# Kernel tuning notes

Hardware: AMD Instinct MI355X
Metric: run time of the kernel (lower is better)

Reference implementation:

```python
import jax, jax.numpy as jnp
import numpy as np

L, S, M, N, E, H = 1024, 1024, 256, 8, 512, 8


def embed_rotary(x, cos, sin):
    # x: [B, T, E]; interleaved rotate-half as in RotaryPositionEncoding.embed_rotary
    x2 = jnp.stack([-x[..., 1::2], x[..., 0::2]], axis=-1).reshape(x.shape)
    return x * cos + x2 * sin


def setup_inputs() -> dict:
    key = jax.random.key(0)
    ks = jax.random.split(key, 12)
    return {
        "query": jax.random.normal(ks[0], (L, N, E), jnp.float32),
        "key": jax.random.normal(ks[1], (S, N, E), jnp.float32),
        "value": jax.random.normal(ks[2], (S, N, E), jnp.float32),
        "in_proj_weight": jax.random.normal(ks[3], (3 * E, E), jnp.float32) / np.sqrt(E).astype(np.float32),
        "in_proj_bias": jnp.zeros((3 * E,), jnp.float32),
        "out_proj_weight": jax.random.normal(ks[4], (E, E), jnp.float32) / np.sqrt(E).astype(np.float32),
        "out_proj_bias": jnp.zeros((E,), jnp.float32),
        "rot_q": jax.random.normal(ks[5], (N, L, E, 2), jnp.float32),
        "rot_k": jax.random.normal(ks[6], (N, S, E, 2), jnp.float32),
        "k_mem": jax.random.normal(ks[7], (M, N, E), jnp.float32),
        "v_mem": jax.random.normal(ks[8], (M, N, E), jnp.float32),
        "gate_attn": jax.random.normal(ks[9], (H,), jnp.float32),
        "mem_mask": jax.random.randint(ks[10], (N, M), 0, 2).astype(bool),
        "num_heads": H,
    }


def reference(query, key, value, in_proj_weight, in_proj_bias, out_proj_weight,
              out_proj_bias, rot_q, rot_k, k_mem, v_mem, gate_attn, mem_mask, num_heads):
    L_, N_, E_ = query.shape
    S_ = key.shape[0]
    H_ = num_heads
    hd = E_ // H_
    scale = float(hd) ** -0.5
    # separate q/k/v projections (qkv not identical path)
    q = query @ in_proj_weight[:E_].T + in_proj_bias[:E_]
    k = key @ in_proj_weight[E_:2 * E_].T + in_proj_bias[E_:2 * E_]
    v = value @ in_proj_weight[2 * E_:].T + in_proj_bias[2 * E_:]
    q = q * scale
    # inline rotary PE (applied in batch-first layout, then back)
    q = embed_rotary(q.transpose(1, 0, 2), rot_q[..., 0], rot_q[..., 1]).transpose(1, 0, 2)
    k = embed_rotary(k.transpose(1, 0, 2), rot_k[..., 0], rot_k[..., 1]).transpose(1, 0, 2)
    qh = q.reshape(L_, N_, H_, hd).transpose(1, 2, 0, 3)  # [N,H,L,hd]
    kh = k.reshape(S_, N_, H_, hd).transpose(1, 2, 0, 3)  # [N,H,S,hd]
    vh = v.reshape(S_, N_, H_, hd).transpose(1, 2, 0, 3)
    scores = jnp.einsum('nhld,nhsd->nhls', qh, kh)
    # slot-competition: softmax over queries (slots), then renormalize over keys
    w = jax.nn.softmax(scores, axis=2) + 1e-8
    w = w / w.sum(axis=-1, keepdims=True)
    attn = jnp.einsum('nhls,nhsd->nhld', w, vh)
    # memorizing-transformer style memory K/V branch with sigmoid head gating
    Mm = k_mem.shape[0]
    km = k_mem.reshape(Mm, N_, H_, hd).transpose(1, 2, 0, 3)  # [N,H,M,hd]
    vm = v_mem.reshape(Mm, N_, H_, hd).transpose(1, 2, 0, 3)
    sm = jnp.einsum('nhld,nhmd->nhlm', qh, km)
    sm = jnp.where(mem_mask[:, None, None, :], -1e9, sm)  # additive -inf mask
    wm = jax.nn.softmax(sm, axis=-1)
    om = jnp.einsum('nhlm,nhmd->nhld', wm, vm)
    gate = jax.nn.sigmoid(gate_attn)[None, :, None, None]  # [1,H,1,1]
    attn = gate * om + (1.0 - gate) * attn
    out = attn.transpose(2, 0, 1, 3).reshape(L_, N_, E_)  # back to [L,N,E]
    return out @ out_proj_weight.T + out_proj_bias
```

## Files before the change

### kernel.cpp

```cpp
#include <hip/hip_runtime.h>
#include <hip/hip_bf16.h>

typedef __hip_bfloat16 bf16;
typedef __bf16 bf16x8 __attribute__((ext_vector_type(8)));
typedef float f32x4 __attribute__((ext_vector_type(4)));

#define LQ 1024
#define SK 1024
#define MMEM 256
#define NB 8
#define EE 512
#define NH 8
#define HD 64
#define NBH 64

__device__ inline __bf16 tobf(float f) {
  __hip_bfloat16 h = __float2bfloat16(f);
  return *reinterpret_cast<__bf16*>(&h);
}
__device__ inline float bf2f(__bf16 x) {
  unsigned short u; __builtin_memcpy(&u, &x, 2);
  unsigned int v = (unsigned int)u << 16;
  float f; __builtin_memcpy(&f, &v, 4);
  return f;
}
__device__ inline f32x4 MFMA(bf16x8 a, bf16x8 b, f32x4 c) {
  return __builtin_amdgcn_mfma_f32_16x16x32_bf16(a, b, c, 0, 0, 0);
}

__device__ inline void gload_lds16(const bf16* g, void* l) {
  __builtin_amdgcn_global_load_lds(
      (const __attribute__((address_space(1))) void*)g,
      (__attribute__((address_space(3))) void*)l, 16, 0, 0);
}

__device__ inline bf16x8 load8(const float* p) {
  float4 a = *(const float4*)p;
  float4 b = *(const float4*)(p + 4);
  bf16x8 r;
  r[0] = tobf(a.x); r[1] = tobf(a.y); r[2] = tobf(a.z); r[3] = tobf(a.w);
  r[4] = tobf(b.x); r[5] = tobf(b.y); r[6] = tobf(b.z); r[7] = tobf(b.w);
  return r;
}

#define CVT_T0 524288
#define CVT_T3 98304
#define CVT_T4 32768
__global__ __launch_bounds__(256) void convert5(
    const float* __restrict__ q, const float* __restrict__ k,
    const float* __restrict__ v, const float* __restrict__ w,
    const float* __restrict__ o, bf16* __restrict__ qc, bf16* __restrict__ kc,
    bf16* __restrict__ vc, bf16* __restrict__ wc, bf16* __restrict__ oc)
{
  long long t = (long long)blockIdx.x * 256 + threadIdx.x;
  const float* src; bf16* dst; long long idx;
  if (t < CVT_T0)               { src = q; dst = qc; idx = t; }
  else if (t < 2 * CVT_T0)      { src = k; dst = kc; idx = t - CVT_T0; }
  else if (t < 3 * CVT_T0)      { src = v; dst = vc; idx = t - 2 * CVT_T0; }
  else if (t < 3 * CVT_T0 + CVT_T3) { src = w; dst = wc; idx = t - 3 * CVT_T0; }
  else                          { src = o; dst = oc; idx = t - 3 * CVT_T0 - CVT_T3; }
  *(bf16x8*)(dst + idx * 8) = load8(src + idx * 8);
}

__global__ __launch_bounds__(256) void gemm_proj3(
    const bf16* __restrict__ qc, const bf16* __restrict__ kc,
    const bf16* __restrict__ vc, const bf16* __restrict__ ipwb,
    const float* __restrict__ ipb, bf16* __restrict__ pq,
    bf16* __restrict__ pk, bf16* __restrict__ v_raw)
{
  __shared__ __align__(16) char smem[33792];
  __bf16* As = (__bf16*)smem;
  __bf16* Bs = (__bf16*)(smem + 16384);
  const int z = blockIdx.z;
  const bf16* A = (z == 0) ? qc : (z == 1) ? kc : vc;
  const bf16* W = ipwb + (long long)z * EE * EE;
  const float* bias = ipb + z * EE;
  const float alpha = (z == 0) ? 0.125f : 1.f;
  const int bid2 = blockIdx.y * gridDim.x + blockIdx.x;
  const int xcd = bid2 & 7, sub = bid2 >> 3;
  const int by = (xcd << 3) + (sub >> 2);
  const int bx = sub & 3;
  const int tm0 = by << 7, tn0 = bx << 7;
  const int t = threadIdx.x;
  const int wave = t >> 6, lane = t & 63;
  const int wrow0 = (wave & 1) << 6, wcol0 = (wave >> 1) << 6;
  const int m16 = lane & 15, quad = lane >> 4;

  const f32x4 zero = {0.f, 0.f, 0.f, 0.f};
  f32x4 acc[4][4];
#pragma unroll
  for (int mi = 0; mi < 4; ++mi)
#pragma unroll
    for (int ni = 0; ni < 4; ++ni) acc[mi][ni] = zero;

  const bf16* Ab = A + (long long)tm0 * EE;
  const bf16* Bb = W + (long long)tn0 * EE;
  const int ob_u = wave << 10;

  for (int k0 = 0; k0 < EE; k0 += 64) {
#pragma unroll
    for (int c = 0; c < 4; ++c) {
      int ob = (c << 12) + ob_u;
      int obl = ob + (lane << 4);
      int row = obl >> 7;
      int ce = (obl & 127) >> 1;
      gload_lds16(Ab + (long long)row * EE + k0 + ce, smem + ob);
      gload_lds16(Bb + (long long)row * EE + k0 + ce, smem + 16384 + ob);
    }
    __syncthreads();
#pragma unroll
    for (int kh = 0; kh < 2; ++kh) {
      bf16x8 av[4], bv[4];
#pragma unroll
      for (int i = 0; i < 4; ++i) {
        av[i] = *(bf16x8*)(As + ((wrow0 + (i << 4) + m16) << 6) + (kh << 5) + (quad << 3));
        bv[i] = *(bf16x8*)(Bs + ((wcol0 + (i << 4) + m16) << 6) + (kh << 5) + (quad << 3));
      }
#pragma unroll
      for (int mi = 0; mi < 4; ++mi)
#pragma unroll
        for (int ni = 0; ni < 4; ++ni)
          acc[mi][ni] = MFMA(av[mi], bv[ni], acc[mi][ni]);
    }
    __syncthreads();
  }

  __bf16 (*Cs)[132] = (__bf16(*)[132])smem;
#pragma unroll
  for (int mi = 0; mi < 4; ++mi)
#pragma unroll
    for (int ni = 0; ni < 4; ++ni) {
      int col = wcol0 + (ni << 4) + m16;
      float bv = bias[tn0 + col];
#pragma unroll
      for (int r = 0; r < 4; ++r)
        Cs[wrow0 + (mi << 4) + (quad << 2) + r][col] =
            tobf((acc[mi][ni][r] + bv) * alpha);
    }
  __syncthreads();
  bf16* O = (z == 0) ? pq : (z == 1) ? pk : v_raw;
  const int crow = t >> 1, ch0 = (t & 1) << 6;
  long long gb = (long long)(tm0 + crow) * EE + tn0 + ch0;
#pragma unroll
  for (int j = 0; j < 64; j += 8)
    *(uint4*)(O + gb + j) = *(uint4*)&Cs[crow][ch0 + j];
}

__global__ __launch_bounds__(256) void rotary_kernel(
    const bf16* __restrict__ pq, const bf16* __restrict__ pk,
    const float* __restrict__ rot_q, const float* __restrict__ rot_k,
    bf16* __restrict__ Qh, bf16* __restrict__ Kh)
{
  const bf16* src = blockIdx.y ? pk : pq;
  const float* rot = blockIdx.y ? rot_k : rot_q;
  bf16* dst = blockIdx.y ? Kh : Qh;
  const int t = threadIdx.x;
  const int row = (blockIdx.x << 2) + (t >> 6);
  const int e0 = (t & 63) << 3;
  const int l = row >> 3, n = row & 7;
  bf16x8 x = *(const bf16x8*)(src + (long long)row * EE + e0);
  const float* rp = rot + ((((long long)n * LQ + l) * EE + e0) << 1);
  __bf16 vals[8];
#pragma unroll
  for (int j = 0; j < 8; j += 2) {
    float4 cs4 = *(const float4*)(rp + (j << 1));
    float x0 = bf2f(x[j]);
    float x1 = bf2f(x[j + 1]);
    vals[j]     = tobf(x0 * cs4.x - x1 * cs4.y);
    vals[j + 1] = tobf(x1 * cs4.z + x0 * cs4.w);
  }
  const int h = e0 >> 6, d0 = e0 & 63;
  *(uint4*)(dst + (((long long)(n * NH + h) * LQ + l) * HD + d0)) = *(uint4*)vals;
}

__global__ __launch_bounds__(256) void colsum_kernel(
    const bf16* __restrict__ Qh, const bf16* __restrict__ Kh,
    float* __restrict__ csum)
{
  __shared__ __align__(16) __bf16 Ks[64][72];
  __shared__ __align__(16) __bf16 Qd[2][64][72];
  __shared__ float cpart[64][2];
  const int bid = blockIdx.y * gridDim.x + blockIdx.x;
  const int xcd = bid & 7, sub = bid >> 3;
  const int b = (xcd << 3) + (sub >> 4);
  const int st0 = (sub & 15) << 6;
  const int t = threadIdx.x;
  const int lrow = t >> 2, lcol = (t & 3) << 4;
  const int wave = t >> 6, lane = t & 63;
  const int wm = (wave & 1) << 5, wn = (wave >> 1) << 5;
  const int m16 = lane & 15, quad = lane >> 4;

  const bf16* qbase = Qh + ((long long)b * LQ + lrow) * HD + lcol;
  {
    const bf16* kp = Kh + ((long long)b * SK + st0 + lrow) * HD + lcol;
    *(bf16x8*)&Ks[lrow][lcol] = *(const bf16x8*)kp;
    *(bf16x8*)&Ks[lrow][lcol + 8] = *(const bf16x8*)(kp + 8);
    *(bf16x8*)&Qd[0][lrow][lcol] = *(const bf16x8*)qbase;
    *(bf16x8*)&Qd[0][lrow][lcol + 8] = *(const bf16x8*)(qbase + 8);
  }
  __syncthreads();
  bf16x8 bk[2][2];
#pragma unroll
  for (int ni = 0; ni < 2; ++ni)
#pragma unroll
    for (int kh = 0; kh < 2; ++kh)
      bk[ni][kh] = *(bf16x8*)&Ks[wn + (ni << 4) + m16][(kh << 5) + (quad << 3)];

  const f32x4 zero = {0.f, 0.f, 0.f, 0.f};
  float colp[2] = {0.f, 0.f};
  int cur = 0;
  for (int lt = 0; lt < 16; ++lt) {
    bf16x8 qr0, qr1;
    if (lt < 15) {
      const bf16* qp = qbase + (long long)((lt + 1) << 6) * HD;
      qr0 = *(const bf16x8*)qp;
      qr1 = *(const bf16x8*)(qp + 8);
    }
    f32x4 s00 = zero, s01 = zero, s10 = zero, s11 = zero;
    __builtin_amdgcn_s_setprio(1);
#pragma unroll
    for (int kh = 0; kh < 2; ++kh) {
      bf16x8 a0 = *(bf16x8*)&Qd[cur][wm + m16][(kh << 5) + (quad << 3)];
      bf16x8 a1 = *(bf16x8*)&Qd[cur][wm + 16 + m16][(kh << 5) + (quad << 3)];
      s00 = MFMA(a0, bk[0][kh], s00);
      s01 = MFMA(a0, bk[1][kh], s01);
      s10 = MFMA(a1, bk[0][kh], s10);
      s11 = MFMA(a1, bk[1][kh], s11);
    }
    __builtin_amdgcn_s_setprio(0);
    f32x4 sacc[2][2] = {{s00, s01}, {s10, s11}};
#pragma unroll
    for (int mi = 0; mi < 2; ++mi)
#pragma unroll
      for (int ni = 0; ni < 2; ++ni)
#pragma unroll
        for (int r = 0; r < 4; ++r)
          colp[ni] += __expf(sacc[mi][ni][r]);
    if (lt < 15) {
      *(bf16x8*)&Qd[cur ^ 1][lrow][lcol] = qr0;
      *(bf16x8*)&Qd[cur ^ 1][lrow][lcol + 8] = qr1;
    }
    __syncthreads();
    cur ^= 1;
  }
  for (int ni = 0; ni < 2; ++ni) {
    float v = colp[ni];
    v += __shfl_down(v, 32, 64);
    v += __shfl_down(v, 16, 64);
    if (quad == 0) cpart[wn + (ni << 4) + m16][wm >> 5] = v;
  }
  __syncthreads();
  if (t < 64) csum[b * SK + st0 + t] = cpart[t][0] + cpart[t][1];
}

__global__ __launch_bounds__(256) void vsum_kernel(
    const bf16* __restrict__ Vt, float* __restrict__ Vsum)
{
  int wid = blockIdx.x * 4 + (threadIdx.x >> 6);
  int lane = threadIdx.x & 63;
  const bf16* p = Vt + (long long)wid * SK + lane * 16;
  float s = 0.f;
  bf16x8 v0 = *(const bf16x8*)p;
  bf16x8 v1 = *(const bf16x8*)(p + 8);
#pragma unroll
  for (int j = 0; j < 8; ++j) s += bf2f(v0[j]) + bf2f(v1[j]);
  for (int off = 32; off; off >>= 1) s += __shfl_down(s, off, 64);
  if (lane == 0) Vsum[wid] = s;
}

__global__ __launch_bounds__(256) void attn_fused(
    const bf16* __restrict__ Qh, const bf16* __restrict__ Kh,
    const bf16* __restrict__ Vt, const bf16* __restrict__ km,
    const bf16* __restrict__ vmt, const float* __restrict__ csum,
    const float* __restrict__ Vsum, const int* __restrict__ mask,
    const float* __restrict__ gate, bf16* __restrict__ comb)
{
  __shared__ __align__(16) __bf16 Kd[2][64][72];
  __shared__ __align__(16) __bf16 Vd[2][64][72];
  __shared__ __align__(16) __bf16 Ps[4096];
  __shared__ __align__(16) float rcs[SK];
  __shared__ __align__(16) float mskf[MMEM];
  __shared__ float rpa[64][2];
  __shared__ float rpm[64][2];
  const int bid = blockIdx.y * gridDim.x + blockIdx.x;
  const int xcd = bid & 7, sub = bid >> 3;
  const int b = (xcd << 3) + (sub >> 4);
  const int tm0 = (sub & 15) << 6;
  const int n = b >> 3, h = b & 7;
  const int t = threadIdx.x;
  const int lrow = t >> 2, lcol = (t & 3) << 4;
  const int wave = t >> 6, lane = t & 63;
  const int wm = (wave & 1) << 5, wn = (wave >> 1) << 5;
  const int m16 = lane & 15, quad = lane >> 4;
  const int swz = (m16 & 7) << 4;

#pragma unroll
  for (int i = 0; i < 4; ++i)
    rcs[t + i * 256] = 1.f / csum[b * SK + t + i * 256];
  mskf[t] = mask[n * MMEM + t] ? 0.f : 1.f;
  {
    const bf16* qp = Qh + ((long long)b * LQ + tm0 + lrow) * HD + lcol;
    *(bf16x8*)&Kd[0][lrow][lcol] = *(const bf16x8*)qp;
    *(bf16x8*)&Kd[0][lrow][lcol + 8] = *(const bf16x8*)(qp + 8);
  }
  __syncthreads();
  bf16x8 aq[2][2];
#pragma unroll
  for (int li = 0; li < 2; ++li)
#pragma unroll
    for (int kh = 0; kh < 2; ++kh)
      aq[li][kh] = *(bf16x8*)&Kd[0][wm + (li << 4) + m16][(kh << 5) + (quad << 3)];

  const bf16* kbase_m = km + ((long long)b * MMEM + lrow) * HD + lcol;
  const bf16* vbase_m = vmt + ((long long)b * HD + lrow) * MMEM + lcol;
  {
    bf16x8 k0 = *(const bf16x8*)kbase_m;
    bf16x8 k1 = *(const bf16x8*)(kbase_m + 8);
    bf16x8 v0 = *(const bf16x8*)vbase_m;
    bf16x8 v1 = *(const bf16x8*)(vbase_m + 8);
    *(bf16x8*)&Kd[1][lrow][lcol] = k0;
    *(bf16x8*)&Kd[1][lrow][lcol + 8] = k1;
    *(bf16x8*)&Vd[1][lrow][lcol] = v0;
    *(bf16x8*)&Vd[1][lrow][lcol + 8] = v1;
  }
  __syncthreads();

  const f32x4 zero = {0.f, 0.f, 0.f, 0.f};
  f32x4 m00 = zero, m01 = zero, m10 = zero, m11 = zero;
  float rsm[2] = {0.f, 0.f};
  int cur = 1;
  for (int mt = 0; mt < 4; ++mt) {
    bf16x8 kr0, kr1, vr0, vr1;
    if (mt < 3) {
      const bf16* kp = kbase_m + (long long)((mt + 1) << 6) * HD;
      const bf16* vp = vbase_m + ((mt + 1) << 6);
      kr0 = *(const bf16x8*)kp;
      kr1 = *(const bf16x8*)(kp + 8);
      vr0 = *(const bf16x8*)vp;
      vr1 = *(const bf16x8*)(vp + 8);
    }
    f32x4 s00 = zero, s01 = zero, s10 = zero, s11 = zero;
    __builtin_amdgcn_s_setprio(1);
#pragma unroll
    for (int kh = 0; kh < 2; ++kh) {
      bf16x8 ak0 = *(bf16x8*)&Kd[cur][wn + m16][(kh << 5) + (quad << 3)];
      bf16x8 ak1 = *(bf16x8*)&Kd[cur][wn + 16 + m16][(kh << 5) + (quad << 3)];
      s00 = MFMA(ak0, aq[0][kh], s00);
      s01 = MFMA(ak0, aq[1][kh], s01);
      s10 = MFMA(ak1, aq[0][kh], s10);
      s11 = MFMA(ak1, aq[1][kh], s11);
    }
    __builtin_amdgcn_s_setprio(0);
    {
      char* pA = (char*)Ps + (wm + m16) * 128;
      char* pB = (char*)Ps + (wm + 16 + m16) * 128;
#pragma unroll
      for (int si = 0; si < 2; ++si) {
        int sloc = wn + (si << 4) + (quad << 2);
        f32x4 mf4 = *(const f32x4*)&mskf[(mt << 6) + sloc];
        f32x4 sA = si ? s10 : s00;
        f32x4 sB = si ? s11 : s01;
        __bf16 vA[4], vB[4];
#pragma unroll
        for (int r = 0; r < 4; ++r) {
          float pa = __expf(sA[r]) * mf4[r];
          rsm[0] += pa; vA[r] = tobf(pa);
          float pb = __expf(sB[r]) * mf4[r];
          rsm[1] += pb; vB[r] = tobf(pb);
        }
        int sbyte = (sloc << 1) ^ swz;
        *(uint2*)(pA + sbyte) = *(uint2*)vA;
        *(uint2*)(pB + sbyte) = *(uint2*)vB;
      }
    }
    __syncthreads();
    if (mt < 3) {
      *(bf16x8*)&Kd[cur ^ 1][lrow][lcol] = kr0;
      *(bf16x8*)&Kd[cur ^ 1][lrow][lcol + 8] = kr1;
      *(bf16x8*)&Vd[cur ^ 1][lrow][lcol] = vr0;
      *(bf16x8*)&Vd[cur ^ 1][lrow][lcol + 8] = vr1;
    }
    __builtin_amdgcn_s_setprio(1);
#pragma unroll
    for (int kh = 0; kh < 2; ++kh) {
      int sb = (kh << 6) + (quad << 4);
      bf16x8 ap0 = *(bf16x8*)((char*)Ps + (wm + m16) * 128 + (sb ^ swz));
      bf16x8 ap1 = *(bf16x8*)((char*)Ps + (wm + 16 + m16) * 128 + (sb ^ swz));
      bf16x8 bv0 = *(bf16x8*)&Vd[cur][wn + m16][(kh << 5) + (quad << 3)];
      bf16x8 bv1 = *(bf16x8*)&Vd[cur][wn + 16 + m16][(kh << 5) + (quad << 3)];
      m00 = MFMA(ap0, bv0, m00);
      m01 = MFMA(ap0, bv1, m01);
      m10 = MFMA(ap1, bv0, m10);
      m11 = MFMA(ap1, bv1, m11);
    }
    __builtin_amdgcn_s_setprio(0);
    __syncthreads();
    cur ^= 1;
  }

  f32x4 o00 = zero, o01 = zero, o10 = zero, o11 = zero;
  float rsa[2] = {0.f, 0.f};
  const bf16* kbase = Kh + ((long long)b * SK + lrow) * HD + lcol;
  const bf16* vbase = Vt + ((long long)b * HD + lrow) * SK + lcol;
  {
    bf16x8 k0 = *(const bf16x8*)kbase;
    bf16x8 k1 = *(const bf16x8*)(kbase + 8);
    bf16x8 v0 = *(const bf16x8*)vbase;
    bf16x8 v1 = *(const bf16x8*)(vbase + 8);
    *(bf16x8*)&Kd[1][lrow][lcol] = k0;
    *(bf16x8*)&Kd[1][lrow][lcol + 8] = k1;
    *(bf16x8*)&Vd[1][lrow][lcol] = v0;
    *(bf16x8*)&Vd[1][lrow][lcol + 8] = v1;
  }
  __syncthreads();
  cur = 1;
  for (int st = 0; st < 16; ++st) {
    bf16x8 kr0, kr1, vr0, vr1;
    if (st < 15) {
      const bf16* kp = kbase + (long long)((st + 1) << 6) * HD;
      const bf16* vp = vbase + ((st + 1) << 6);
      kr0 = *(const bf16x8*)kp;
      kr1 = *(const bf16x8*)(kp + 8);
      vr0 = *(const bf16x8*)vp;
      vr1 = *(const bf16x8*)(vp + 8);
    }
    f32x4 s00 = zero, s01 = zero, s10 = zero, s11 = zero;
    __builtin_amdgcn_s_setprio(1);
#pragma unroll
    for (int kh = 0; kh < 2; ++kh) {
      bf16x8 ak0 = *(bf16x8*)&Kd[cur][wn + m16][(kh << 5) + (quad << 3)];
      bf16x8 ak1 = *(bf16x8*)&Kd[cur][wn + 16 + m16][(kh << 5) + (quad << 3)];
      s00 = MFMA(ak0, aq[0][kh], s00);
      s01 = MFMA(ak0, aq[1][kh], s01);
      s10 = MFMA(ak1, aq[0][kh], s10);
      s11 = MFMA(ak1, aq[1][kh], s11);
    }
    __builtin_amdgcn_s_setprio(0);
    {
      char* pA = (char*)Ps + (wm + m16) * 128;
      char* pB = (char*)Ps + (wm + 16 + m16) * 128;
#pragma unroll
      for (int si = 0; si < 2; ++si) {
        int sloc = wn + (si << 4) + (quad << 2);
        f32x4 rc4 = *(const f32x4*)&rcs[(st << 6) + sloc];
        f32x4 sA = si ? s10 : s00;
        f32x4 sB = si ? s11 : s01;
        __bf16 vA[4], vB[4];
#pragma unroll
        for (int r = 0; r < 4; ++r) {
          float pa = __expf(sA[r]) * rc4[r];
          rsa[0] += pa; vA[r] = tobf(pa);
          float pb = __expf(sB[r]) * rc4[r];
          rsa[1] += pb; vB[r] = tobf(pb);
        }
        int sbyte = (sloc << 1) ^ swz;
        *(uint2*)(pA + sbyte) = *(uint2*)vA;
        *(uint2*)(pB + sbyte) = *(uint2*)vB;
      }
    }
    __syncthreads();
    if (st < 15) {
      *(bf16x8*)&Kd[cur ^ 1][lrow][lcol] = kr0;
      *(bf16x8*)&Kd[cur ^ 1][lrow][lcol + 8] = kr1;
      *(bf16x8*)&Vd[cur ^ 1][lrow][lcol] = vr0;
      *(bf16x8*)&Vd[cur ^ 1][lrow][lcol + 8] = vr1;
    }
    __builtin_amdgcn_s_setprio(1);
#pragma unroll
    for (int kh = 0; kh < 2; ++kh) {
      int sb = (kh << 6) + (quad << 4);
      bf16x8 ap0 = *(bf16x8*)((char*)Ps + (wm + m16) * 128 + (sb ^ swz));
      bf16x8 ap1 = *(bf16x8*)((char*)Ps + (wm + 16 + m16) * 128 + (sb ^ swz));
      bf16x8 bv0 = *(bf16x8*)&Vd[cur][wn + m16][(kh << 5) + (quad << 3)];
      bf16x8 bv1 = *(bf16x8*)&Vd[cur][wn + 16 + m16][(kh << 5) + (quad << 3)];
      o00 = MFMA(ap0, bv0, o00);
      o01 = MFMA(ap0, bv1, o01);
      o10 = MFMA(ap1, bv0, o10);
      o11 = MFMA(ap1, bv1, o11);
    }
    __builtin_amdgcn_s_setprio(0);
    __syncthreads();
    cur ^= 1;
  }

#pragma unroll
  for (int li = 0; li < 2; ++li) {
    float va = rsa[li];
    va += __shfl_xor(va, 16, 64);
    va += __shfl_xor(va, 32, 64);
    float vm = rsm[li];
    vm += __shfl_xor(vm, 16, 64);
    vm += __shfl_xor(vm, 32, 64);
    if (quad == 0) {
      rpa[wm + (li << 4) + m16][wn >> 5] = va;
      rpm[wm + (li << 4) + m16][wn >> 5] = vm;
    }
  }
  __syncthreads();

  const float* vs = Vsum + b * HD;
  const float g = 1.f / (1.f + __expf(-gate[h]));
  f32x4 oacc[2][2] = {{o00, o01}, {o10, o11}};
  f32x4 macc[2][2] = {{m00, m01}, {m10, m11}};
  for (int mi = 0; mi < 2; ++mi)
    for (int ni = 0; ni < 2; ++ni) {
      int col = wn + (ni << 4) + m16;
      float vsc = 1e-8f * vs[col];
      for (int r = 0; r < 4; ++r) {
        int row = wm + (mi << 4) + (quad << 2) + r;
        float ra = rpa[row][0] + rpa[row][1];
        float rm = rpm[row][0] + rpm[row][1];
        float oa = (oacc[mi][ni][r] + vsc) / (ra + (float)SK * 1e-8f);
        float om = macc[mi][ni][r] / rm;
        Kd[0][row][col] = tobf(g * om + (1.f - g) * oa);
      }
    }
  __syncthreads();
  uint4 u0 = *(uint4*)&Kd[0][lrow][lcol];
  uint4 u1 = *(uint4*)&Kd[0][lrow][lcol + 8];
  long long gb = ((long long)b * LQ + tm0 + lrow) * HD + lcol;
  *(uint4*)(comb + gb) = u0;
  *(uint4*)(comb + gb + 8) = u1;
}

__global__ __launch_bounds__(256) void gemm_out(
    const bf16* __restrict__ comb, const bf16* __restrict__ opwb,
    const float* __restrict__ opb, float* __restrict__ out)
{
  __shared__ __align__(16) char smem[32768];
  __bf16* As = (__bf16*)smem;
  __bf16* Bs = (__bf16*)(smem + 16384);
  const int bid2 = blockIdx.y * gridDim.x + blockIdx.x;
  const int xcd = bid2 & 7, sub = bid2 >> 3;
  const int by = (xcd << 3) + (sub >> 2);
  const int bx = sub & 3;
  const int tm0 = by << 7, tn0 = bx << 7;
  const int t = threadIdx.x;
  const int wave = t >> 6, lane = t & 63;
  const int wrow0 = (wave & 1) << 6, wcol0 = (wave >> 1) << 6;
  const int m16 = lane & 15, quad = lane >> 4;

  const f32x4 zero = {0.f, 0.f, 0.f, 0.f};
  f32x4 acc[4][4];
#pragma unroll
  for (int mi = 0; mi < 4; ++mi)
#pragma unroll
    for (int ni = 0; ni < 4; ++ni) acc[mi][ni] = zero;

  const bf16* Bb = opwb + (long long)tn0 * EE;
  const int ob_u = wave << 10;

  for (int k0 = 0; k0 < EE; k0 += 64) {
    const int h = k0 >> 6;
#pragma unroll
    for (int c = 0; c < 4; ++c) {
      int ob = (c << 12) + ob_u;
      int obl = ob + (lane << 4);
      int row = obl >> 7;
      int ce = (obl & 127) >> 1;
      int arow = tm0 + row;
      int l = arow >> 3, nn = arow & 7;
      gload_lds16(comb + (((long long)(nn * NH + h) * LQ + l) * HD + ce),
                  smem + ob);
      gload_lds16(Bb + (long long)row * EE + k0 + ce, smem + 16384 + ob);
    }
    __syncthreads();
#pragma unroll
    for (int kh = 0; kh < 2; ++kh) {
      bf16x8 av[4], bv[4];
#pragma unroll
      for (int i = 0; i < 4; ++i) {
        av[i] = *(bf16x8*)(As + ((wrow0 + (i << 4) + m16) << 6) + (kh << 5) + (quad << 3));
        bv[i] = *(bf16x8*)(Bs + ((wcol0 + (i << 4) + m16) << 6) + (kh << 5) + (quad << 3));
      }
#pragma unroll
      for (int mi = 0; mi < 4; ++mi)
#pragma unroll
        for (int ni = 0; ni < 4; ++ni)
          acc[mi][ni] = MFMA(av[mi], bv[ni], acc[mi][ni]);
    }
    __syncthreads();
  }

#pragma unroll
  for (int mi = 0; mi < 4; ++mi)
#pragma unroll
    for (int ni = 0; ni < 4; ++ni) {
      int col = tn0 + wcol0 + (ni << 4) + m16;
      float bv = opb[col];
      int row0 = tm0 + wrow0 + (mi << 4) + (quad << 2);
#pragma unroll
      for (int r = 0; r < 4; ++r)
        out[(long long)(row0 + r) * EE + col] = acc[mi][ni][r] + bv;
    }
}

__global__ __launch_bounds__(256) void v_transpose(
    const bf16* __restrict__ raw, bf16* __restrict__ Vt)
{
  __shared__ __align__(16) __bf16 Ts[64][72];
  const int bh = blockIdx.y;
  const int n = bh >> 3, h = bh & 7;
  const int s0 = blockIdx.x << 6;
  const int t = threadIdx.x;
  const int i = t >> 2, c0 = (t & 3) << 4;
  const bf16* rp = raw + ((long long)(s0 + i) * NB + n) * EE + h * HD + c0;
  *(bf16x8*)&Ts[i][c0] = *(const bf16x8*)rp;
  *(bf16x8*)&Ts[i][c0 + 8] = *(const bf16x8*)(rp + 8);
  __syncthreads();
  const int d = t >> 2, j0 = (t & 3) << 4;
  __bf16 vals[16];
#pragma unroll
  for (int j = 0; j < 16; ++j) vals[j] = Ts[j0 + j][d];
  bf16* wp = Vt + ((long long)bh * HD + d) * SK + s0 + j0;
  *(uint4*)wp = *(uint4*)&vals[0];
  *(uint4*)(wp + 8) = *(uint4*)&vals[8];
}

__global__ __launch_bounds__(256) void mem_prep(
    const float* __restrict__ k_mem, const float* __restrict__ v_mem,
    bf16* __restrict__ km, bf16* __restrict__ vmt)
{
  __shared__ __align__(16) __bf16 Ts[64][72];
  const int bh = blockIdx.y;
  const int n = bh >> 3, h = bh & 7;
  const int m0 = blockIdx.x << 6;
  const int t = threadIdx.x;
  const int i = t >> 2, c0 = (t & 3) << 4;
  const float* kp = k_mem + ((long long)(m0 + i) * NB + n) * EE + h * HD + c0;
  const float* vp = v_mem + ((long long)(m0 + i) * NB + n) * EE + h * HD + c0;
  bf16x8 kv0 = load8(kp), kv1 = load8(kp + 8);
  bf16x8 vv0 = load8(vp), vv1 = load8(vp + 8);
  bf16* kw = km + ((long long)bh * MMEM + m0 + i) * HD + c0;
  *(bf16x8*)kw = kv0;
  *(bf16x8*)(kw + 8) = kv1;
  *(bf16x8*)&Ts[i][c0] = vv0;
  *(bf16x8*)&Ts[i][c0 + 8] = vv1;
  __syncthreads();
  const int d = t >> 2, j0 = (t & 3) << 4;
  __bf16 vals[16];
#pragma unroll
  for (int j = 0; j < 16; ++j) vals[j] = Ts[j0 + j][d];
  bf16* wp = vmt + ((long long)bh * HD + d) * MMEM + m0 + j0;
  *(uint4*)wp = *(uint4*)&vals[0];
  *(uint4*)(wp + 8) = *(uint4*)&vals[8];
}

extern "C" void kernel_launch(void* const* d_in, const int* in_sizes, int n_in,
                              void* d_out, int out_size, void* d_ws, size_t ws_size,
                              hipStream_t stream) {
  const float* query = (const float*)d_in[0];
  const float* key   = (const float*)d_in[1];
  const float* value = (const float*)d_in[2];
  const float* ipw   = (const float*)d_in[3];
  const float* ipb   = (const float*)d_in[4];
  const float* opw   = (const float*)d_in[5];
  const float* opb   = (const float*)d_in[6];
  const float* rot_q = (const float*)d_in[7];
  const float* rot_k = (const float*)d_in[8];
  const float* k_mem = (const float*)d_in[9];
  const float* v_mem = (const float*)d_in[10];
  const float* gate  = (const float*)d_in[11];
  const int*  mask   = (const int*)d_in[12];
  float* out = (float*)d_out;

  char* w = (char*)d_ws;
  size_t off = 0;
  auto carve = [&](size_t bytes) -> char* {
    char* p = w + off;
    off += (bytes + 255) & ~(size_t)255;
    return p;
  };
  bf16* qc    = (bf16*)carve((size_t)LQ * NB * EE * 2);
  bf16* kc    = (bf16*)carve((size_t)SK * NB * EE * 2);
  bf16* vc    = (bf16*)carve((size_t)SK * NB * EE * 2);
  bf16* ipwb  = (bf16*)carve((size_t)3 * EE * EE * 2);
  bf16* opwb  = (bf16*)carve((size_t)EE * EE * 2);
  bf16* v_raw = (bf16*)carve((size_t)SK * NB * EE * 2);
  bf16* Qh    = (bf16*)carve((size_t)NBH * LQ * HD * 2);
  bf16* Kh    = (bf16*)carve((size_t)NBH * SK * HD * 2);
  bf16* Vt    = (bf16*)carve((size_t)NBH * HD * SK * 2);
  bf16* km    = (bf16*)carve((size_t)NBH * MMEM * HD * 2);
  bf16* vmt   = (bf16*)carve((size_t)NBH * HD * MMEM * 2);
  float* csum = (float*)carve((size_t)NBH * SK * 4);
  float* Vsum = (float*)carve((size_t)NBH * HD * 4);
  bf16* comb  = (bf16*)carve((size_t)NBH * LQ * HD * 2);
  bf16* pkbuf = (bf16*)carve((size_t)NBH * LQ * HD * 2);
  if (off > ws_size) {
    hipMemsetAsync(d_out, 0, (size_t)out_size * 4, stream);
    return;
  }
  bf16* pq = comb;
  bf16* pk = pkbuf;

  convert5<<<(3 * CVT_T0 + CVT_T3 + CVT_T4) / 256, 256, 0, stream>>>(
      query, key, value, ipw, opw, qc, kc, vc, ipwb, opwb);

  gemm_proj3<<<dim3(EE / 128, (LQ * NB) / 128, 3), 256, 0, stream>>>(
      qc, kc, vc, ipwb, ipb, pq, pk, v_raw);

  rotary_kernel<<<dim3((LQ * NB) / 4, 2), 256, 0, stream>>>(
      pq, pk, rot_q, rot_k, Qh, Kh);

  v_transpose<<<dim3(SK / 64, NBH), 256, 0, stream>>>(v_raw, Vt);
  vsum_kernel<<<(NBH * HD) / 4, 256, 0, stream>>>(Vt, Vsum);
  mem_prep<<<dim3(MMEM / 64, NBH), 256, 0, stream>>>(k_mem, v_mem, km, vmt);

  colsum_kernel<<<dim3(SK / 64, NBH), 256, 0, stream>>>(Qh, Kh, csum);

  attn_fused<<<dim3(LQ / 64, NBH), 256, 0, stream>>>(
      Qh, Kh, Vt, km, vmt, csum, Vsum, mask, gate, comb);

  gemm_out<<<dim3(4, 64), 256, 0, stream>>>(comb, opwb, opb, out);
}
```

Measured before the change: 301.3 us.

## Fold log2e into Q scale, widen colsum tiles, fuse V-sum into transpose

Multiplies the query scale by log2(e) so every softmax exponent can use exp2f instead of __expf. The column-sum kernel now handles 128 keys per block, holding K fragments in registers and streaming Q tiles into swizzled LDS with direct global-to-LDS loads. This halves the number of blocks and the repeated Q reads. The separate vsum kernel is removed; V column sums are accumulated with atomics during the V transpose, which needs a memset of the sum buffer first and adds atomic traffic.

```diff
diff --git a/kernel.cpp b/kernel.cpp
--- a/kernel.cpp
+++ b/kernel.cpp
@@ -75,7 +75,7 @@
   const bf16* A = (z == 0) ? qc : (z == 1) ? kc : vc;
   const bf16* W = ipwb + (long long)z * EE * EE;
   const float* bias = ipb + z * EE;
-  const float alpha = (z == 0) ? 0.125f : 1.f;
+  const float alpha = (z == 0) ? 0.1803368801f : 1.f;
   const int bid2 = blockIdx.y * gridDim.x + blockIdx.x;
   const int xcd = bid2 & 7, sub = bid2 >> 3;
   const int by = (xcd << 3) + (sub >> 2);
@@ -177,95 +177,100 @@
     const bf16* __restrict__ Qh, const bf16* __restrict__ Kh,
     float* __restrict__ csum)
 {
-  __shared__ __align__(16) __bf16 Ks[64][72];
-  __shared__ __align__(16) __bf16 Qd[2][64][72];
-  __shared__ float cpart[64][2];
+  __shared__ __align__(16) char QdB[16384];
+  __shared__ float cpart[128][2];
   const int bid = blockIdx.y * gridDim.x + blockIdx.x;
   const int xcd = bid & 7, sub = bid >> 3;
-  const int b = (xcd << 3) + (sub >> 4);
-  const int st0 = (sub & 15) << 6;
+  const int b = (xcd << 3) + (sub >> 3);
+  const int st0 = (sub & 7) << 7;
   const int t = threadIdx.x;
-  const int lrow = t >> 2, lcol = (t & 3) << 4;
   const int wave = t >> 6, lane = t & 63;
   const int wm = (wave & 1) << 5, wn = (wave >> 1) << 5;
   const int m16 = lane & 15, quad = lane >> 4;
-
-  const bf16* qbase = Qh + ((long long)b * LQ + lrow) * HD + lcol;
-  {
-    const bf16* kp = Kh + ((long long)b * SK + st0 + lrow) * HD + lcol;
-    *(bf16x8*)&Ks[lrow][lcol] = *(const bf16x8*)kp;
-    *(bf16x8*)&Ks[lrow][lcol + 8] = *(const bf16x8*)(kp + 8);
-    *(bf16x8*)&Qd[0][lrow][lcol] = *(const bf16x8*)qbase;
-    *(bf16x8*)&Qd[0][lrow][lcol + 8] = *(const bf16x8*)(qbase + 8);
-  }
-  __syncthreads();
-  bf16x8 bk[2][2];
-#pragma unroll
-  for (int ni = 0; ni < 2; ++ni)
-#pragma unroll
-    for (int kh = 0; kh < 2; ++kh)
-      bk[ni][kh] = *(bf16x8*)&Ks[wn + (ni << 4) + m16][(kh << 5) + (quad << 3)];
+  const int swz = (m16 & 7) << 4;
+
+  bf16x8 bk[2][2][2];
+#pragma unroll
+  for (int g = 0; g < 2; ++g)
+#pragma unroll
+    for (int ni = 0; ni < 2; ++ni)
+#pragma unroll
+      for (int kh = 0; kh < 2; ++kh)
+        bk[g][ni][kh] = *(const bf16x8*)(
+            Kh + ((long long)b * SK + st0 + (g << 6) + wn + (ni << 4) + m16) * HD
+               + (kh << 5) + (quad << 3));
+
+  int ldsoff[2]; const bf16* qsrc[2];
+#pragma unroll
+  for (int c = 0; c < 2; ++c) {
+    int tb = (wave << 11) + (c << 10) + (lane << 4);
+    int row = tb >> 7, cb = tb & 127;
+    int srcb = cb ^ ((row & 7) << 4);
+    ldsoff[c] = (wave << 11) + (c << 10);
+    qsrc[c] = Qh + ((long long)b * LQ + row) * HD + (srcb >> 1);
+  }
+#pragma unroll
+  for (int c = 0; c < 2; ++c) gload_lds16(qsrc[c], QdB + ldsoff[c]);
+  __syncthreads();
 
   const f32x4 zero = {0.f, 0.f, 0.f, 0.f};
-  float colp[2] = {0.f, 0.f};
+  float colp[2][2] = {{0.f, 0.f}, {0.f, 0.f}};
   int cur = 0;
   for (int lt = 0; lt < 16; ++lt) {
-    bf16x8 qr0, qr1;
     if (lt < 15) {
-      const bf16* qp = qbase + (long long)((lt + 1) << 6) * HD;
-      qr0 = *(const bf16x8*)qp;
-      qr1 = *(const bf16x8*)(qp + 8);
-    }
-    f32x4 s00 = zero, s01 = zero, s10 = zero, s11 = zero;
+#pragma unroll
+      for (int c = 0; c < 2; ++c)
+        gload_lds16(qsrc[c] + (long long)(lt + 1) * 64 * HD,
+                    QdB + ((cur ^ 1) << 13) + ldsoff[c]);
+    }
+    bf16x8 a0k[2], a1k[2];
+#pragma unroll
+    for (int kh = 0; kh < 2; ++kh) {
+      int byt = ((kh << 6) + (quad << 4)) ^ swz;
+      a0k[kh] = *(bf16x8*)(QdB + (cur << 13) + (wm + m16) * 128 + byt);
+      a1k[kh] = *(bf16x8*)(QdB + (cur << 13) + (wm + 16 + m16) * 128 + byt);
+    }
+    f32x4 s[2][2][2];
+#pragma unroll
+    for (int g = 0; g < 2; ++g)
+#pragma unroll
+      for (int mi = 0; mi < 2; ++mi)
+#pragma unroll
+        for (int ni = 0; ni < 2; ++ni) s[g][mi][ni] = zero;
     __builtin_amdgcn_s_setprio(1);
 #pragma unroll
-    for (int kh = 0; kh < 2; ++kh) {
-      bf16x8 a0 = *(bf16x8*)&Qd[cur][wm + m16][(kh << 5) + (quad << 3)];
-      bf16x8 a1 = *(bf16x8*)&Qd[cur][wm + 16 + m16][(kh << 5) + (quad << 3)];
-      s00 = MFMA(a0, bk[0][kh], s00);
-      s01 = MFMA(a0, bk[1][kh], s01);
-      s10 = MFMA(a1, bk[0][kh], s10);
-      s11 = MFMA(a1, bk[1][kh], s11);
-    }
+    for (int g = 0; g < 2; ++g)
+#pragma unroll
+      for (int kh = 0; kh < 2; ++kh) {
+        s[g][0][0] = MFMA(a0k[kh], bk[g][0][kh], s[g][0][0]);
+        s[g][0][1] = MFMA(a0k[kh], bk[g][1][kh], s[g][0][1]);
+        s[g][1][0] = MFMA(a1k[kh], bk[g][0][kh], s[g][1][0]);
+        s[g][1][1] = MFMA(a1k[kh], bk[g][1][kh], s[g][1][1]);
+      }
     __builtin_amdgcn_s_setprio(0);
-    f32x4 sacc[2][2] = {{s00, s01}, {s10, s11}};
-#pragma unroll
-    for (int mi = 0; mi < 2; ++mi)
-#pragma unroll
-      for (int ni = 0; ni < 2; ++ni)
-#pragma unroll
-        for (int r = 0; r < 4; ++r)
-          colp[ni] += __expf(sacc[mi][ni][r]);
-    if (lt < 15) {
-      *(bf16x8*)&Qd[cur ^ 1][lrow][lcol] = qr0;
-      *(bf16x8*)&Qd[cur ^ 1][lrow][lcol + 8] = qr1;
-    }
+#pragma unroll
+    for (int g = 0; g < 2; ++g)
+#pragma unroll
+      for (int mi = 0; mi < 2; ++mi)
+#pragma unroll
+        for (int ni = 0; ni < 2; ++ni)
+#pragma unroll
+          for (int r = 0; r < 4; ++r)
+            colp[g][ni] += exp2f(s[g][mi][ni][r]);
     __syncthreads();
     cur ^= 1;
   }
-  for (int ni = 0; ni < 2; ++ni) {
-    float v = colp[ni];
-    v += __shfl_down(v, 32, 64);
-    v += __shfl_down(v, 16, 64);
-    if (quad == 0) cpart[wn + (ni << 4) + m16][wm >> 5] = v;
-  }
-  __syncthreads();
-  if (t < 64) csum[b * SK + st0 + t] = cpart[t][0] + cpart[t][1];
-}
-
-__global__ __launch_bounds__(256) void vsum_kernel(
-    const bf16* __restrict__ Vt, float* __restrict__ Vsum)
-{
-  int wid = blockIdx.x * 4 + (threadIdx.x >> 6);
-  int lane = threadIdx.x & 63;
-  const bf16* p = Vt + (long long)wid * SK + lane * 16;
-  float s = 0.f;
-  bf16x8 v0 = *(const bf16x8*)p;
-  bf16x8 v1 = *(const bf16x8*)(p + 8);
-#pragma unroll
-  for (int j = 0; j < 8; ++j) s += bf2f(v0[j]) + bf2f(v1[j]);
-  for (int off = 32; off; off >>= 1) s += __shfl_down(s, off, 64);
-  if (lane == 0) Vsum[wid] = s;
+#pragma unroll
+  for (int g = 0; g < 2; ++g)
+#pragma unroll
+    for (int ni = 0; ni < 2; ++ni) {
+      float v = colp[g][ni];
+      v += __shfl_down(v, 32, 64);
+      v += __shfl_down(v, 16, 64);
+      if (quad == 0) cpart[(g << 6) + wn + (ni << 4) + m16][wm >> 5] = v;
+    }
+  __syncthreads();
+  if (t < 128) csum[b * SK + st0 + t] = cpart[t][0] + cpart[t][1];
 }
 
 __global__ __launch_bounds__(256) void attn_fused(
@@ -280,8 +285,6 @@
   __shared__ __align__(16) __bf16 Ps[4096];
   __shared__ __align__(16) float rcs[SK];
   __shared__ __align__(16) float mskf[MMEM];
-  __shared__ float rpa[64][2];
-  __shared__ float rpm[64][2];
   const int bid = blockIdx.y * gridDim.x + blockIdx.x;
   const int xcd = bid & 7, sub = bid >> 3;
   const int b = (xcd << 3) + (sub >> 4);
@@ -293,6 +296,8 @@
   const int wm = (wave & 1) << 5, wn = (wave >> 1) << 5;
   const int m16 = lane & 15, quad = lane >> 4;
   const int swz = (m16 & 7) << 4;
+  __shared__ float rpa[64][2];
+  __shared__ float rpm[64][2];
 
 #pragma unroll
   for (int i = 0; i < 4; ++i)
@@ -363,9 +368,9 @@
         __bf16 vA[4], vB[4];
 #pragma unroll
         for (int r = 0; r < 4; ++r) {
-          float pa = __expf(sA[r]) * mf4[r];
+          float pa = exp2f(sA[r]) * mf4[r];
           rsm[0] += pa; vA[r] = tobf(pa);
-          float pb = __expf(sB[r]) * mf4[r];
+          float pb = exp2f(sB[r]) * mf4[r];
           rsm[1] += pb; vB[r] = tobf(pb);
         }
         int sbyte = (sloc << 1) ^ swz;
@@ -448,9 +453,9 @@
         __bf16 vA[4], vB[4];
 #pragma unroll
         for (int r = 0; r < 4; ++r) {
-          float pa = __expf(sA[r]) * rc4[r];
+          float pa = exp2f(sA[r]) * rc4[r];
           rsa[0] += pa; vA[r] = tobf(pa);
-          float pb = __expf(sB[r]) * rc4[r];
+          float pb = exp2f(sB[r]) * rc4[r];
           rsa[1] += pb; vB[r] = tobf(pb);
         }
         int sbyte = (sloc << 1) ^ swz;
@@ -596,7 +601,8 @@
 }
 
 __global__ __launch_bounds__(256) void v_transpose(
-    const bf16* __restrict__ raw, bf16* __restrict__ Vt)
+    const bf16* __restrict__ raw, bf16* __restrict__ Vt,
+    float* __restrict__ Vsum)
 {
   __shared__ __align__(16) __bf16 Ts[64][72];
   const int bh = blockIdx.y;
@@ -610,11 +616,15 @@
   __syncthreads();
   const int d = t >> 2, j0 = (t & 3) << 4;
   __bf16 vals[16];
-#pragma unroll
-  for (int j = 0; j < 16; ++j) vals[j] = Ts[j0 + j][d];
+  float part = 0.f;
+#pragma unroll
+  for (int j = 0; j < 16; ++j) { vals[j] = Ts[j0 + j][d]; part += bf2f(vals[j]); }
   bf16* wp = Vt + ((long long)bh * HD + d) * SK + s0 + j0;
   *(uint4*)wp = *(uint4*)&vals[0];
   *(uint4*)(wp + 8) = *(uint4*)&vals[8];
+  part += __shfl_xor(part, 1, 64);
+  part += __shfl_xor(part, 2, 64);
+  if ((t & 3) == 0) atomicAdd(&Vsum[bh * HD + d], part);
 }
 
 __global__ __launch_bounds__(256) void mem_prep(
@@ -695,6 +705,7 @@
 
   convert5<<<(3 * CVT_T0 + CVT_T3 + CVT_T4) / 256, 256, 0, stream>>>(
       query, key, value, ipw, opw, qc, kc, vc, ipwb, opwb);
+  hipMemsetAsync(Vsum, 0, (size_t)NBH * HD * 4, stream);
 
   gemm_proj3<<<dim3(EE / 128, (LQ * NB) / 128, 3), 256, 0, stream>>>(
       qc, kc, vc, ipwb, ipb, pq, pk, v_raw);
@@ -702,11 +713,10 @@
   rotary_kernel<<<dim3((LQ * NB) / 4, 2), 256, 0, stream>>>(
       pq, pk, rot_q, rot_k, Qh, Kh);
 
-  v_transpose<<<dim3(SK / 64, NBH), 256, 0, stream>>>(v_raw, Vt);
-  vsum_kernel<<<(NBH * HD) / 4, 256, 0, stream>>>(Vt, Vsum);
+  v_transpose<<<dim3(SK / 64, NBH), 256, 0, stream>>>(v_raw, Vt, Vsum);
   mem_prep<<<dim3(MMEM / 64, NBH), 256, 0, stream>>>(k_mem, v_mem, km, vmt);
 
-  colsum_kernel<<<dim3(SK / 64, NBH), 256, 0, stream>>>(Qh, Kh, csum);
+  colsum_kernel<<<dim3(SK / 128, NBH), 256, 0, stream>>>(Qh, Kh, csum);
 
   attn_fused<<<dim3(LQ / 64, NBH), 256, 0, stream>>>(
       Qh, Kh, Vt, km, vmt, csum, Vsum, mask, gate, comb);
```

Measured after the change: 343.5 us. 14.0% more time.
